# Performance work log

Measured on AMD Instinct MI355X. Metric: run time of the kernel, lower is better.

Reference implementation:

```python
import jax, jax.numpy as jnp
import numpy as np

H = 16  # num_heads


def _sinusoidal_positions(n_pos, d, dtype=jnp.float32):
    half = d // 2
    freqs = 1.0 / 10000 ** (jnp.arange(0, half, dtype=dtype) / float(half))
    pos = jnp.arange(n_pos, dtype=dtype)[:, None]
    angles = pos * freqs[None, :]
    emb = jnp.concatenate([jnp.sin(angles), jnp.cos(angles)], axis=-1)
    if d % 2 == 1:
        emb = jnp.pad(emb, ((0, 0), (0, 1)))
    return emb.astype(dtype)


def setup_inputs() -> dict:
    key = jax.random.key(0)
    B, M, C = 64, 2048, 1024
    D = C // H
    ks = jax.random.split(key, 12)
    s = 1.0 / np.sqrt(C)
    return {
        "x": jax.random.normal(ks[0], (B, C), jnp.float32),
        "mem": jax.random.normal(ks[1], (B, M, C), jnp.float32),
        "Wq": jax.random.normal(ks[2], (C, C), jnp.float32) * s,
        "bq": jnp.zeros((C,), jnp.float32),
        "Wk": jax.random.normal(ks[3], (C, C), jnp.float32) * s,
        "bk": jnp.zeros((C,), jnp.float32),
        "Wv": jax.random.normal(ks[4], (C, C), jnp.float32) * s,
        "bv": jnp.zeros((C,), jnp.float32),
        "u_bias": jax.random.normal(ks[5], (H, D), jnp.float32) * 0.02,
        "v_bias": jax.random.normal(ks[6], (H, D), jnp.float32) * 0.02,
        "Wo": jax.random.normal(ks[7], (C, C), jnp.float32) * s,
        "bo": jnp.zeros((C,), jnp.float32),
    }


def reference(x, mem, Wq, bq, Wk, bk, Wv, bv, u_bias, v_bias, Wo, bo):
    B, C = x.shape
    D = C // H
    M = mem.shape[1]
    L = M + 1
    cat = jnp.concatenate([mem, x[:, None, :]], axis=1)  # (B, L, C)
    q = (x @ Wq + bq).reshape(B, H, D)
    k = (cat @ Wk + bk).reshape(B, L, H, D)
    v = (cat @ Wv + bv).reshape(B, L, H, D)
    r = _sinusoidal_positions(L, D)[::-1, :]  # (L, D), reversed
    scale = 1.0 / jnp.sqrt(jnp.float32(D))
    ac = jnp.einsum('bhd,blhd->bhl', q + u_bias[None, :, :], k)
    bd = jnp.einsum('bhd,ld->bhl', q + v_bias[None, :, :], r)
    attn = jax.nn.softmax((ac + bd) * scale, axis=-1)
    out = jnp.einsum('bhl,blhd->bhd', attn, v).reshape(B, C)
    return out @ Wo + bo
```

## Files before the change

### kernel.cpp

```cpp
#include <hip/hip_runtime.h>
#include <hip/hip_bf16.h>
#include <math.h>

#define B   64
#define C   1024
#define HH  16
#define DD  64
#define MM  2048
#define LL  2049
#define SCALE 0.125f
#define NCHC 9
#define CHC  228

__global__ __launch_bounds__(256) void k_gemm(
    const float* __restrict__ A, int a_row_stride, int a_bx_off,
    const float* __restrict__ W, float* __restrict__ P) {
  __shared__ __attribute__((aligned(16))) float a_s[64 * 132];
  __shared__ __attribute__((aligned(16))) float b_s[128 * 68];
  int t = threadIdx.x;
  int jt = blockIdx.x, kc = blockIdx.y;
  const float* Ab = A + (size_t)jt * a_bx_off;
  int k0 = kc * 128;
  for (int idx = t; idx < 2048; idx += 256) {
    int bb = idx >> 5, f4 = idx & 31;
    float4 v = *(const float4*)&Ab[(size_t)bb * a_row_stride + k0 + 4 * f4];
    *(float4*)&a_s[bb * 132 + 4 * f4] = v;
  }
  for (int idx = t; idx < 2048; idx += 256) {
    int kk = idx >> 4, f4 = idx & 15;
    float4 v = *(const float4*)&W[(size_t)(k0 + kk) * 1024 + jt * 64 + 4 * f4];
    *(float4*)&b_s[kk * 68 + 4 * f4] = v;
  }
  __syncthreads();
  int j0 = (t & 15) * 4, b0 = (t >> 4) * 4;
  float4 acc[4];
#pragma unroll
  for (int i = 0; i < 4; ++i) acc[i] = make_float4(0.f, 0.f, 0.f, 0.f);
  for (int k = 0; k < 128; k += 4) {
    float4 w0 = *(const float4*)&b_s[(k + 0) * 68 + j0];
    float4 w1 = *(const float4*)&b_s[(k + 1) * 68 + j0];
    float4 w2 = *(const float4*)&b_s[(k + 2) * 68 + j0];
    float4 w3 = *(const float4*)&b_s[(k + 3) * 68 + j0];
#pragma unroll
    for (int i = 0; i < 4; ++i) {
      float4 av = *(const float4*)&a_s[(b0 + i) * 132 + k];
      acc[i].x += av.x * w0.x + av.y * w1.x + av.z * w2.x + av.w * w3.x;
      acc[i].y += av.x * w0.y + av.y * w1.y + av.z * w2.y + av.w * w3.y;
      acc[i].z += av.x * w0.z + av.y * w1.z + av.z * w2.z + av.w * w3.z;
      acc[i].w += av.x * w0.w + av.y * w1.w + av.z * w2.w + av.w * w3.w;
    }
  }
  size_t ob = (size_t)kc * 65536 + jt * 64;
#pragma unroll
  for (int i = 0; i < 4; ++i)
    *(float4*)&P[ob + (size_t)(b0 + i) * 1024 + j0] = acc[i];
}

__global__ __launch_bounds__(256) void k_reduce_qp(
    const float* __restrict__ P, const float* __restrict__ bq,
    const float* __restrict__ u, const float* __restrict__ v,
    float* __restrict__ qu, float* __restrict__ qv) {
  int idx = blockIdx.x * 256 + threadIdx.x;
  int b = idx >> 8, f4 = idx & 255;
  size_t off = (size_t)b * 1024 + 4 * f4;
  float4 s = *(const float4*)&P[off];
#pragma unroll
  for (int kc = 1; kc < 8; ++kc) {
    float4 t4 = *(const float4*)&P[(size_t)kc * 65536 + off];
    s.x += t4.x; s.y += t4.y; s.z += t4.z; s.w += t4.w;
  }
  float4 bb = *(const float4*)&bq[4 * f4];
  s.x += bb.x; s.y += bb.y; s.z += bb.z; s.w += bb.w;
  float4 uu = *(const float4*)&u[4 * f4];
  float4 vv = *(const float4*)&v[4 * f4];
  float4 o1 = make_float4(s.x + uu.x, s.y + uu.y, s.z + uu.z, s.w + uu.w);
  float4 o2 = make_float4(s.x + vv.x, s.y + vv.y, s.z + vv.z, s.w + vv.w);
  *(float4*)&qu[off] = o1;
  *(float4*)&qv[off] = o2;
}

__global__ __launch_bounds__(256) void k_reduce1(
    const float* __restrict__ P, const float* __restrict__ bias,
    float* __restrict__ out) {
  int idx = blockIdx.x * 256 + threadIdx.x;
  int b = idx >> 8, f4 = idx & 255;
  size_t off = (size_t)b * 1024 + 4 * f4;
  float4 s = *(const float4*)&P[off];
#pragma unroll
  for (int kc = 1; kc < 8; ++kc) {
    float4 t4 = *(const float4*)&P[(size_t)kc * 65536 + off];
    s.x += t4.x; s.y += t4.y; s.z += t4.z; s.w += t4.w;
  }
  float4 bb = *(const float4*)&bias[4 * f4];
  s.x += bb.x; s.y += bb.y; s.z += bb.z; s.w += bb.w;
  *(float4*)&out[off] = s;
}

__global__ __launch_bounds__(256) void k_wtilde(
    const float* __restrict__ qu, const float* __restrict__ Wk,
    float* __restrict__ wt) {
  __shared__ __attribute__((aligned(16))) float a_s[64 * 68];
  __shared__ __attribute__((aligned(16))) float w_s[64 * 68];
  int t = threadIdx.x, ct = blockIdx.x, h = blockIdx.y;
  for (int idx = t; idx < 1024; idx += 256) {
    int bb = idx >> 4, f4 = idx & 15;
    *(float4*)&a_s[bb * 68 + 4 * f4] =
        *(const float4*)&qu[(size_t)bb * 1024 + h * 64 + 4 * f4];
  }
  for (int idx = t; idx < 1024; idx += 256) {
    int cc = idx >> 4, f4 = idx & 15;
    *(float4*)&w_s[cc * 68 + 4 * f4] =
        *(const float4*)&Wk[(size_t)(ct * 64 + cc) * 1024 + h * 64 + 4 * f4];
  }
  __syncthreads();
  int c0 = (t & 15) * 4, b0 = (t >> 4) * 4;
  float acc[4][4] = {};
  for (int d = 0; d < 64; d += 4) {
    float4 w0 = *(const float4*)&w_s[(c0 + 0) * 68 + d];
    float4 w1 = *(const float4*)&w_s[(c0 + 1) * 68 + d];
    float4 w2 = *(const float4*)&w_s[(c0 + 2) * 68 + d];
    float4 w3 = *(const float4*)&w_s[(c0 + 3) * 68 + d];
#pragma unroll
    for (int i = 0; i < 4; ++i) {
      float4 av = *(const float4*)&a_s[(b0 + i) * 68 + d];
      acc[i][0] += av.x * w0.x + av.y * w0.y + av.z * w0.z + av.w * w0.w;
      acc[i][1] += av.x * w1.x + av.y * w1.y + av.z * w1.z + av.w * w1.w;
      acc[i][2] += av.x * w2.x + av.y * w2.y + av.z * w2.z + av.w * w2.w;
      acc[i][3] += av.x * w3.x + av.y * w3.y + av.z * w3.z + av.w * w3.w;
    }
  }
#pragma unroll
  for (int i = 0; i < 4; ++i) {
    float4 o = make_float4(acc[i][0], acc[i][1], acc[i][2], acc[i][3]);
    *(float4*)&wt[(size_t)((b0 + i) * 16 + h) * 1024 + ct * 64 + c0] = o;
  }
}

__global__ void k_rtab(float* __restrict__ rtab) {
  int idx = blockIdx.x * 256 + threadIdx.x;
  if (idx >= LL * 64) return;
  int l = idx >> 6, d = idx & 63;
  float p = (float)(LL - 1 - l);
  int dd = d & 31;
  float f = 1.0f / powf(10000.0f, (float)dd * (1.0f / 32.0f));
  float a = p * f;
  rtab[idx] = (d < 32) ? sinf(a) : cosf(a);
}

__global__ __launch_bounds__(256) void k_bd(
    const float* __restrict__ qv, const float* __restrict__ rtab,
    float* __restrict__ bd) {
  __shared__ __attribute__((aligned(16))) float rt_s[128 * 68];
  int t = threadIdx.x, ch = blockIdx.x, b = blockIdx.y;
  int l0 = ch * 128;
  int nrows = min(128, LL - l0);
  for (int idx = t; idx < nrows * 16; idx += 256) {
    int r = idx >> 4, d4 = idx & 15;
    *(float4*)&rt_s[r * 68 + 4 * d4] =
        *(const float4*)&rtab[(size_t)(l0 + r) * 64 + 4 * d4];
  }
  __syncthreads();
  for (int idx = t; idx < 16 * 128; idx += 256) {
    int h = idx >> 7, r = idx & 127;
    if (r < nrows) {
      const float* qh = &qv[(size_t)b * 1024 + h * 64];
      const float* rr = &rt_s[r * 68];
      float s = 0.f;
#pragma unroll
      for (int d4 = 0; d4 < 16; ++d4) {
        float4 rv = *(const float4*)&rr[4 * d4];
        float4 qq = *(const float4*)&qh[4 * d4];
        s += rv.x * qq.x + rv.y * qq.y + rv.z * qq.z + rv.w * qq.w;
      }
      bd[(size_t)(b * 16 + h) * LL + l0 + r] = s;
    }
  }
}

__global__ __launch_bounds__(256) void k_logits(
    const float* __restrict__ x, const float* __restrict__ mem,
    const float* __restrict__ wt, const float* __restrict__ bd,
    float* __restrict__ logits) {
  __shared__ float red_s[8 * 68];
  int t = threadIdx.x;
  int lane = t & 63, w = t >> 6;
  int b = blockIdx.y, ch = blockIdx.x;
  int l0 = ch * 128, lend = min(LL, l0 + 128);
  int c_off = w * 256 + lane * 4;
  float4 wr[16];
#pragma unroll
  for (int h = 0; h < 16; ++h)
    wr[h] = *(const float4*)&wt[(size_t)(b * 16 + h) * 1024 + c_off];
  const float* xrow = &x[(size_t)b * 1024 + c_off];
  const float* memb = &mem[(size_t)b * MM * 1024 + c_off];
  bool b5 = (lane & 32) != 0, b4 = (lane & 16) != 0;
  bool b3 = (lane & 8) != 0, b2 = (lane & 4) != 0;
  int hl = lane >> 2;

  for (int g0 = l0; g0 < lend; g0 += 8) {
    int nr = min(8, lend - g0);
    float4 rb[8];
#pragma unroll
    for (int r = 0; r < 8; ++r) {
      int l = g0 + r;
      rb[r] = *(const float4*)((l < MM) ? &memb[(size_t)l * 1024] : xrow);
    }
#pragma unroll
    for (int r = 0; r < 8; ++r) {
      if (r < nr) {
        float4 rv = rb[r];
        float p[16];
#pragma unroll
        for (int h = 0; h < 16; ++h)
          p[h] = rv.x * wr[h].x + rv.y * wr[h].y + rv.z * wr[h].z +
                 rv.w * wr[h].w;
        float q[8];
#pragma unroll
        for (int i = 0; i < 8; ++i) {
          float send = b5 ? p[i] : p[i + 8];
          float keep = b5 ? p[i + 8] : p[i];
          q[i] = keep + __shfl_xor(send, 32, 64);
        }
        float r2[4];
#pragma unroll
        for (int i = 0; i < 4; ++i) {
          float send = b4 ? q[i] : q[i + 4];
          float keep = b4 ? q[i + 4] : q[i];
          r2[i] = keep + __shfl_xor(send, 16, 64);
        }
        float s2[2];
#pragma unroll
        for (int i = 0; i < 2; ++i) {
          float send = b3 ? r2[i] : r2[i + 2];
          float keep = b3 ? r2[i + 2] : r2[i];
          s2[i] = keep + __shfl_xor(send, 8, 64);
        }
        float send4 = b2 ? s2[0] : s2[1];
        float keep4 = b2 ? s2[1] : s2[0];
        float u = keep4 + __shfl_xor(send4, 4, 64);
        u += __shfl_xor(u, 1, 64);
        u += __shfl_xor(u, 2, 64);
        if ((lane & 3) == 0) red_s[r * 68 + w * 16 + hl] = u;
      }
    }
    __syncthreads();
    if (t < 128) {
      int r8 = t & 7, h = t >> 3;
      if (r8 < nr) {
        float s = red_s[r8 * 68 + h] + red_s[r8 * 68 + 16 + h] +
                  red_s[r8 * 68 + 32 + h] + red_s[r8 * 68 + 48 + h];
        int l = g0 + r8;
        size_t o = (size_t)(b * 16 + h) * LL + l;
        logits[o] = (s + bd[o]) * SCALE;
      }
    }
    __syncthreads();
  }
}

__global__ __launch_bounds__(256) void k_softmax(float* __restrict__ logits) {
  __shared__ float red[8];
  int t = threadIdx.x;
  size_t base = (size_t)blockIdx.x * LL;
  float rv[9];
  float m = -1e30f;
#pragma unroll
  for (int k = 0; k < 9; ++k) {
    int i = t + k * 256;
    rv[k] = (i < LL) ? logits[base + i] : -1e30f;
    m = fmaxf(m, rv[k]);
  }
#pragma unroll
  for (int s = 1; s < 64; s <<= 1) m = fmaxf(m, __shfl_xor(m, s, 64));
  if ((t & 63) == 0) red[t >> 6] = m;
  __syncthreads();
  m = fmaxf(fmaxf(red[0], red[1]), fmaxf(red[2], red[3]));
  float sum = 0.f;
#pragma unroll
  for (int k = 0; k < 9; ++k) {
    int i = t + k * 256;
    float e = __expf(rv[k] - m);
    rv[k] = e;
    if (i < LL) sum += e;
  }
#pragma unroll
  for (int s = 1; s < 64; s <<= 1) sum += __shfl_xor(sum, s, 64);
  if ((t & 63) == 0) red[4 + (t >> 6)] = sum;
  __syncthreads();
  float inv = 1.0f / (red[4] + red[5] + red[6] + red[7]);
#pragma unroll
  for (int k = 0; k < 9; ++k) {
    int i = t + k * 256;
    if (i < LL) logits[base + i] = rv[k] * inv;
  }
}

__global__ __launch_bounds__(256) void k_ctx(
    const float* __restrict__ x, const float* __restrict__ mem,
    const float* __restrict__ attn, float* __restrict__ part) {
  __shared__ __attribute__((aligned(16))) float att_s[CHC * 20];
  int t = threadIdx.x;
  int lane = t & 63, w = t >> 6;
  int b = blockIdx.y;
  int ch = blockIdx.x >> 2, cq = blockIdx.x & 3;
  int l0 = ch * CHC, lend = min(LL, l0 + CHC);
  int natt = lend - l0;
  int c_off = cq * 256 + lane * 4;
#pragma unroll
  for (int h = 0; h < 16; ++h)
    for (int r = t; r < natt; r += 256)
      att_s[r * 20 + h] = attn[(size_t)(b * 16 + h) * LL + l0 + r];
  __syncthreads();
  float4 acc[16];
#pragma unroll
  for (int i = 0; i < 16; ++i) acc[i] = make_float4(0.f, 0.f, 0.f, 0.f);
  const float* xrow = &x[(size_t)b * 1024 + c_off];
  const float* memb = &mem[(size_t)b * MM * 1024 + c_off];

  for (int g0 = l0 + w * 8; g0 < lend; g0 += 32) {
    int nr = min(8, lend - g0);
    float4 rb[8];
#pragma unroll
    for (int r = 0; r < 8; ++r) {
      int l = g0 + r;
      rb[r] = *(const float4*)((l < MM) ? &memb[(size_t)l * 1024] : xrow);
    }
#pragma unroll
    for (int r = 0; r < 8; ++r) {
      if (r < nr) {
        int ri = g0 + r - l0;
        const float4* a4 = (const float4*)&att_s[ri * 20];
        float4 aA = a4[0], aB = a4[1], aC = a4[2], aD = a4[3];
        float4 rv = rb[r];
#define ACC1(i, s)                                                       \
  acc[i].x += (s) * rv.x; acc[i].y += (s) * rv.y;                        \
  acc[i].z += (s) * rv.z; acc[i].w += (s) * rv.w;
        ACC1(0, aA.x) ACC1(1, aA.y) ACC1(2, aA.z) ACC1(3, aA.w)
        ACC1(4, aB.x) ACC1(5, aB.y) ACC1(6, aB.z) ACC1(7, aB.w)
        ACC1(8, aC.x) ACC1(9, aC.y) ACC1(10, aC.z) ACC1(11, aC.w)
        ACC1(12, aD.x) ACC1(13, aD.y) ACC1(14, aD.z) ACC1(15, aD.w)
#undef ACC1
      }
    }
  }
  __syncthreads();
  float* accb = att_s;
  for (int ww = 0; ww < 4; ++ww) {
    if (w == ww) {
      if (ww == 0) {
#pragma unroll
        for (int h = 0; h < 16; ++h)
          *(float4*)&accb[h * 256 + lane * 4] = acc[h];
      } else {
#pragma unroll
        for (int h = 0; h < 16; ++h) {
          float4 vv = *(const float4*)&accb[h * 256 + lane * 4];
          vv.x += acc[h].x; vv.y += acc[h].y;
          vv.z += acc[h].z; vv.w += acc[h].w;
          *(float4*)&accb[h * 256 + lane * 4] = vv;
        }
      }
    }
    __syncthreads();
  }
  size_t pb = (size_t)((b * NCHC + ch) * 16) * 1024 + cq * 256;
  for (int idx = t; idx < 1024; idx += 256) {
    int h = idx >> 6, c4 = idx & 63;
    *(float4*)&part[pb + (size_t)h * 1024 + 4 * c4] =
        *(const float4*)&accb[h * 256 + 4 * c4];
  }
}

__global__ __launch_bounds__(256) void k_ctxreduce(
    const float* __restrict__ part, float* __restrict__ ctx) {
  int o4 = blockIdx.x * 256 + threadIdx.x;
  size_t o = (size_t)o4 * 4;
  int b = (int)(o >> 14);
  int rem = (int)(o & 16383);
  const float* p = &part[(size_t)b * (NCHC * 16384) + rem];
  float4 s = *(const float4*)p;
#pragma unroll
  for (int chk = 1; chk < NCHC; ++chk) {
    float4 v = *(const float4*)&p[(size_t)chk * 16384];
    s.x += v.x; s.y += v.y; s.z += v.z; s.w += v.w;
  }
  *(float4*)&ctx[o] = s;
}

extern "C" void kernel_launch(void* const* d_in, const int* in_sizes, int n_in,
                              void* d_out, int out_size, void* d_ws,
                              size_t ws_size, hipStream_t stream) {
  const float* x = (const float*)d_in[0];
  const float* mem = (const float*)d_in[1];
  const float* Wq = (const float*)d_in[2];
  const float* bq = (const float*)d_in[3];
  const float* Wk = (const float*)d_in[4];
  const float* Wv = (const float*)d_in[6];
  const float* bv = (const float*)d_in[7];
  const float* u_bias = (const float*)d_in[8];
  const float* v_bias = (const float*)d_in[9];
  const float* Wo = (const float*)d_in[10];
  const float* bo = (const float*)d_in[11];
  float* out = (float*)d_out;

  float* ws = (float*)d_ws;
  float* qu = ws;
  float* qv = qu + 65536;
  float* logits = qv + 65536;
  float* ctx = logits + 2098176;
  float* out1 = ctx + 1048576;
  float* Bb = out1 + 65536;
  float* wt = Bb;
  float* rtab = Bb + 1048576;
  float* bd = Bb + 1179776;
  float* P = Bb + 3277952;
  float* part = Bb;

  k_gemm<<<dim3(16, 8), 256, 0, stream>>>(x, 1024, 0, Wq, P);
  k_rtab<<<dim3(513), 256, 0, stream>>>(rtab);
  k_reduce_qp<<<dim3(64), 256, 0, stream>>>(P, bq, u_bias, v_bias, qu, qv);
  k_wtilde<<<dim3(16, 16), 256, 0, stream>>>(qu, Wk, wt);
  k_bd<<<dim3(17, 64), 256, 0, stream>>>(qv, rtab, bd);
  k_logits<<<dim3(17, 64), 256, 0, stream>>>(x, mem, wt, bd, logits);
  k_softmax<<<dim3(1024), 256, 0, stream>>>(logits);
  k_ctx<<<dim3(36, 64), 256, 0, stream>>>(x, mem, logits, part);
  k_ctxreduce<<<dim3(1024), 256, 0, stream>>>(part, ctx);
  k_gemm<<<dim3(16, 8), 256, 0, stream>>>(ctx, 16384, 1024, Wv, P);
  k_reduce1<<<dim3(64), 256, 0, stream>>>(P, bv, out1);
  k_gemm<<<dim3(16, 8), 256, 0, stream>>>(out1, 1024, 0, Wo, P);
  k_reduce1<<<dim3(64), 256, 0, stream>>>(P, bo, out);
}
```

Baseline: 431.2 us.

## Fuse positional bd term into logits kernel with row-per-thread tiled layout

Replaces the separate bd kernel and the shuffle-reduction logits kernel with one kernel in which each thread owns one key position. Mem/x rows are staged through swizzled shared memory in 32-column chunks, and each thread accumulates all 16 heads against wtilde, which is read as wave-uniform broadcast loads. The bd dot product against the rope table is then added in the epilogue. This drops the bd buffer round trip, the launch, and the cross-lane shuffle reductions, at the cost of fewer blocks (9x64) and more syncs per block.

```diff
diff --git a/kernel.cpp b/kernel.cpp
--- a/kernel.cpp
+++ b/kernel.cpp
@@ -11,6 +11,8 @@
 #define SCALE 0.125f
 #define NCHC 9
 #define CHC  228
+#define L2ROWS 256
+#define L2CK 32
 
 __global__ __launch_bounds__(256) void k_gemm(
     const float* __restrict__ A, int a_row_stride, int a_bx_off,
@@ -147,114 +149,65 @@
   rtab[idx] = (d < 32) ? sinf(a) : cosf(a);
 }
 
-__global__ __launch_bounds__(256) void k_bd(
-    const float* __restrict__ qv, const float* __restrict__ rtab,
-    float* __restrict__ bd) {
-  __shared__ __attribute__((aligned(16))) float rt_s[128 * 68];
-  int t = threadIdx.x, ch = blockIdx.x, b = blockIdx.y;
-  int l0 = ch * 128;
-  int nrows = min(128, LL - l0);
-  for (int idx = t; idx < nrows * 16; idx += 256) {
-    int r = idx >> 4, d4 = idx & 15;
-    *(float4*)&rt_s[r * 68 + 4 * d4] =
-        *(const float4*)&rtab[(size_t)(l0 + r) * 64 + 4 * d4];
-  }
-  __syncthreads();
-  for (int idx = t; idx < 16 * 128; idx += 256) {
-    int h = idx >> 7, r = idx & 127;
-    if (r < nrows) {
-      const float* qh = &qv[(size_t)b * 1024 + h * 64];
-      const float* rr = &rt_s[r * 68];
+__global__ __launch_bounds__(256) void k_logits2(
+    const float* __restrict__ x, const float* __restrict__ mem,
+    const float* __restrict__ wt, const float* __restrict__ qv,
+    const float* __restrict__ rtab, float* __restrict__ logits) {
+  __shared__ __attribute__((aligned(16))) float cat_s[L2ROWS * 36];
+  int t = threadIdx.x;
+  int b = blockIdx.y, ch = blockIdx.x;
+  int l0 = ch * L2ROWS;
+  int myl = l0 + t;
+  int lcl = min(myl, LL - 1);
+  const float* wtb = &wt[(size_t)b * 16384];
+  float acc[16];
+#pragma unroll
+  for (int h = 0; h < 16; ++h) acc[h] = 0.f;
+  int key = (t >> 3) & 7;
+
+  for (int c0 = 0; c0 < 1024; c0 += L2CK) {
+    for (int idx = t; idx < L2ROWS * 8; idx += 256) {
+      int r = idx >> 3, c4 = idx & 7;
+      int l = min(l0 + r, LL - 1);
+      const float* src = (l < MM) ? &mem[((size_t)b * MM + l) * 1024]
+                                  : &x[(size_t)b * 1024];
+      float4 v = *(const float4*)&src[c0 + 4 * c4];
+      int sw = c4 ^ ((r >> 3) & 7);
+      *(float4*)&cat_s[r * 36 + 4 * sw] = v;
+    }
+    __syncthreads();
+    float4 cv[8];
+#pragma unroll
+    for (int k = 0; k < 8; ++k)
+      cv[k] = *(const float4*)&cat_s[t * 36 + 4 * (k ^ key)];
+#pragma unroll 2
+    for (int h = 0; h < 16; ++h) {
+      const float4* wp = (const float4*)&wtb[h * 1024 + c0];
       float s = 0.f;
 #pragma unroll
-      for (int d4 = 0; d4 < 16; ++d4) {
-        float4 rv = *(const float4*)&rr[4 * d4];
-        float4 qq = *(const float4*)&qh[4 * d4];
-        s += rv.x * qq.x + rv.y * qq.y + rv.z * qq.z + rv.w * qq.w;
+      for (int k = 0; k < 8; ++k) {
+        float4 wv = wp[k];
+        s += cv[k].x * wv.x + cv[k].y * wv.y + cv[k].z * wv.z + cv[k].w * wv.w;
       }
-      bd[(size_t)(b * 16 + h) * LL + l0 + r] = s;
-    }
-  }
-}
-
-__global__ __launch_bounds__(256) void k_logits(
-    const float* __restrict__ x, const float* __restrict__ mem,
-    const float* __restrict__ wt, const float* __restrict__ bd,
-    float* __restrict__ logits) {
-  __shared__ float red_s[8 * 68];
-  int t = threadIdx.x;
-  int lane = t & 63, w = t >> 6;
-  int b = blockIdx.y, ch = blockIdx.x;
-  int l0 = ch * 128, lend = min(LL, l0 + 128);
-  int c_off = w * 256 + lane * 4;
-  float4 wr[16];
-#pragma unroll
-  for (int h = 0; h < 16; ++h)
-    wr[h] = *(const float4*)&wt[(size_t)(b * 16 + h) * 1024 + c_off];
-  const float* xrow = &x[(size_t)b * 1024 + c_off];
-  const float* memb = &mem[(size_t)b * MM * 1024 + c_off];
-  bool b5 = (lane & 32) != 0, b4 = (lane & 16) != 0;
-  bool b3 = (lane & 8) != 0, b2 = (lane & 4) != 0;
-  int hl = lane >> 2;
-
-  for (int g0 = l0; g0 < lend; g0 += 8) {
-    int nr = min(8, lend - g0);
-    float4 rb[8];
-#pragma unroll
-    for (int r = 0; r < 8; ++r) {
-      int l = g0 + r;
-      rb[r] = *(const float4*)((l < MM) ? &memb[(size_t)l * 1024] : xrow);
-    }
-#pragma unroll
-    for (int r = 0; r < 8; ++r) {
-      if (r < nr) {
-        float4 rv = rb[r];
-        float p[16];
-#pragma unroll
-        for (int h = 0; h < 16; ++h)
-          p[h] = rv.x * wr[h].x + rv.y * wr[h].y + rv.z * wr[h].z +
-                 rv.w * wr[h].w;
-        float q[8];
-#pragma unroll
-        for (int i = 0; i < 8; ++i) {
-          float send = b5 ? p[i] : p[i + 8];
-          float keep = b5 ? p[i + 8] : p[i];
-          q[i] = keep + __shfl_xor(send, 32, 64);
-        }
-        float r2[4];
-#pragma unroll
-        for (int i = 0; i < 4; ++i) {
-          float send = b4 ? q[i] : q[i + 4];
-          float keep = b4 ? q[i + 4] : q[i];
-          r2[i] = keep + __shfl_xor(send, 16, 64);
-        }
-        float s2[2];
-#pragma unroll
-        for (int i = 0; i < 2; ++i) {
-          float send = b3 ? r2[i] : r2[i + 2];
-          float keep = b3 ? r2[i + 2] : r2[i];
-          s2[i] = keep + __shfl_xor(send, 8, 64);
-        }
-        float send4 = b2 ? s2[0] : s2[1];
-        float keep4 = b2 ? s2[1] : s2[0];
-        float u = keep4 + __shfl_xor(send4, 4, 64);
-        u += __shfl_xor(u, 1, 64);
-        u += __shfl_xor(u, 2, 64);
-        if ((lane & 3) == 0) red_s[r * 68 + w * 16 + hl] = u;
-      }
+      acc[h] += s;
     }
     __syncthreads();
-    if (t < 128) {
-      int r8 = t & 7, h = t >> 3;
-      if (r8 < nr) {
-        float s = red_s[r8 * 68 + h] + red_s[r8 * 68 + 16 + h] +
-                  red_s[r8 * 68 + 32 + h] + red_s[r8 * 68 + 48 + h];
-        int l = g0 + r8;
-        size_t o = (size_t)(b * 16 + h) * LL + l;
-        logits[o] = (s + bd[o]) * SCALE;
-      }
-    }
-    __syncthreads();
+  }
+  float4 rv[16];
+#pragma unroll
+  for (int k = 0; k < 16; ++k)
+    rv[k] = *(const float4*)&rtab[(size_t)lcl * 64 + 4 * k];
+#pragma unroll 2
+  for (int h = 0; h < 16; ++h) {
+    const float4* qp = (const float4*)&qv[(size_t)b * 1024 + h * 64];
+    float s = 0.f;
+#pragma unroll
+    for (int k = 0; k < 16; ++k) {
+      float4 q = qp[k];
+      s += rv[k].x * q.x + rv[k].y * q.y + rv[k].z * q.z + rv[k].w * q.w;
+    }
+    if (myl < LL)
+      logits[(size_t)(b * 16 + h) * LL + myl] = (acc[h] + s) * SCALE;
   }
 }
 
@@ -412,16 +365,14 @@
   float* Bb = out1 + 65536;
   float* wt = Bb;
   float* rtab = Bb + 1048576;
-  float* bd = Bb + 1179776;
-  float* P = Bb + 3277952;
+  float* P = Bb + 1179776;
   float* part = Bb;
 
   k_gemm<<<dim3(16, 8), 256, 0, stream>>>(x, 1024, 0, Wq, P);
   k_rtab<<<dim3(513), 256, 0, stream>>>(rtab);
   k_reduce_qp<<<dim3(64), 256, 0, stream>>>(P, bq, u_bias, v_bias, qu, qv);
   k_wtilde<<<dim3(16, 16), 256, 0, stream>>>(qu, Wk, wt);
-  k_bd<<<dim3(17, 64), 256, 0, stream>>>(qv, rtab, bd);
-  k_logits<<<dim3(17, 64), 256, 0, stream>>>(x, mem, wt, bd, logits);
+  k_logits2<<<dim3(9, 64), 256, 0, stream>>>(x, mem, wt, qv, rtab, logits);
   k_softmax<<<dim3(1024), 256, 0, stream>>>(logits);
   k_ctx<<<dim3(36, 64), 256, 0, stream>>>(x, mem, logits, part);
   k_ctxreduce<<<dim3(1024), 256, 0, stream>>>(part, ctx);
```

After: 587.8 us. +36.3%, slower.
